# Kernel optimization log

Measured on AMD Instinct MI355X. Metric: run time of the kernel, lower is better.

## Reference

```python
import jax, jax.numpy as jnp
import numpy as np

FEATURE_DIM = 1024
HEADS = 16
HEAD_DIM = FEATURE_DIM // HEADS


def setup_inputs() -> dict:
    key = jax.random.key(0)
    ks = jax.random.split(key, 9)
    B, C, T = 4, FEATURE_DIM, 4096
    s = 1.0 / np.sqrt(C)
    inp = {
        "x": jax.random.normal(ks[0], (B, C, T), dtype=jnp.float32),
        "Wq": jax.random.uniform(ks[1], (C, C), jnp.float32, -s, s),
        "bq": jax.random.uniform(ks[2], (C,), jnp.float32, -s, s),
        "Wk": jax.random.uniform(ks[3], (C, C), jnp.float32, -s, s),
        "bk": jax.random.uniform(ks[4], (C,), jnp.float32, -s, s),
        "Wv": jax.random.uniform(ks[5], (C, C), jnp.float32, -s, s),
        "bv": jax.random.uniform(ks[6], (C,), jnp.float32, -s, s),
        "Wo": jax.random.uniform(ks[7], (C, C), jnp.float32, -s, s),
        "bo": jax.random.uniform(ks[8], (C,), jnp.float32, -s, s),
    }
    return inp


def reference(x, Wq, bq, Wk, bk, Wv, bv, Wo, bo):
    B, C, T = x.shape
    H, D = HEADS, HEAD_DIM
    xt = jnp.transpose(x, (0, 2, 1))  # [B, T, C]
    # torch Linear: y = x @ W.T + b
    q = jax.nn.elu(xt @ Wq.T + bq).reshape(B, T, H, D) + 1.0
    k = jax.nn.elu(xt @ Wk.T + bk).reshape(B, T, H, D) + 1.0
    v = (xt @ Wv.T + bv).reshape(B, T, H, D)
    kv = jnp.einsum('bthd,bthe->bhde', k, v)      # [B, H, D, D]
    z = jnp.einsum('bthd,bhd->bth', q, k.sum(axis=1))  # [B, T, H]
    num = jnp.einsum('bthd,bhde->bthe', q, kv)    # [B, T, H, D]
    out = num / (z[..., None] + 1e-6)
    out = out.reshape(B, T, C)
    out = out @ Wo.T + bo  # dropout is identity in eval mode
    return jnp.transpose(out + xt, (0, 2, 1))  # [B, C, T]
```

## Files before the change

### kernel.cpp

```cpp
#include <hip/hip_runtime.h>
#include <hip/hip_bf16.h>
#include <cmath>

typedef unsigned short u16;
typedef unsigned int   u32;

#define BB 4
#define CC 1024
#define TT 4096
#define HH 16
#define DD 64

using bf16x8 = __attribute__((ext_vector_type(8))) __bf16;
using f32x4  = __attribute__((ext_vector_type(4))) float;

union FragU { bf16x8 v; u16 u[8]; };

__device__ __forceinline__ float bf2f(u16 u) {
    union { u32 i; float f; } v; v.i = ((u32)u) << 16; return v.f;
}
__device__ __forceinline__ u16 f2bf(float f) {
    union { float f; u32 i; } v; v.f = f;
    u32 x = v.i;
    return (u16)((x + 0x7fffu + ((x >> 16) & 1u)) >> 16);
}

__device__ __forceinline__ void gl_lds16(const u16* g, u16* l) {
    __builtin_amdgcn_global_load_lds(
        (const __attribute__((address_space(1))) void*)g,
        (__attribute__((address_space(3))) void*)l, 16, 0, 0);
}

__global__ __launch_bounds__(256) void prep_kernel(
    const float* __restrict__ x,
    const float* __restrict__ Wq, const float* __restrict__ Wk,
    const float* __restrict__ Wv, const float* __restrict__ Wo,
    u16* __restrict__ xt, u16* __restrict__ Wcat, u16* __restrict__ Wob,
    float* __restrict__ kvz)
{
    __shared__ u16 tile[64 * 258];
    const int id  = blockIdx.x;
    const int tid = threadIdx.x;

    if (id < 1024) {
        const int t0 = (id & 63) * 64;
        const int c0 = ((id >> 6) & 3) * 256;
        const int b  = id >> 8;
        const float* xb  = x  + (size_t)b * CC * TT;
        u16*         xtb = xt + (size_t)b * TT * CC;
        const int tcol = tid & 63;
        const int rw   = tid >> 6;
        #pragma unroll 8
        for (int p = 0; p < 64; ++p) {
            const int cr = p * 4 + rw;
            tile[tcol * 258 + cr] = f2bf(xb[(size_t)(c0 + cr) * TT + t0 + tcol]);
        }
        __syncthreads();
        const int cp = tid & 127;
        const int th = tid >> 7;
        #pragma unroll 8
        for (int q = 0; q < 32; ++q) {
            const int tr = q * 2 + th;
            const u32 v = *reinterpret_cast<const u32*>(&tile[tr * 258 + cp * 2]);
            *reinterpret_cast<u32*>(&xtb[(size_t)(t0 + tr) * CC + c0 + cp * 2]) = v;
        }
    } else if (id < 5120) {
        const int id2  = id - 1024;
        const int wsel = id2 >> 10;
        const int i    = ((id2 & 1023) * 256 + tid) * 4;
        const float* src = (wsel == 0) ? Wq : (wsel == 1) ? Wk : (wsel == 2) ? Wv : Wo;
        u16* dst = (wsel < 3) ? (Wcat + (size_t)wsel * CC * CC) : Wob;
        const float4 v = *reinterpret_cast<const float4*>(src + i);
        ushort4 o;
        o.x = f2bf(v.x); o.y = f2bf(v.y); o.z = f2bf(v.z); o.w = f2bf(v.w);
        *reinterpret_cast<ushort4*>(dst + i) = o;
    } else {
        const int idx = ((id - 5120) * 256 + tid) * 4;
        *reinterpret_cast<float4*>(&kvz[idx]) = (float4){0.f, 0.f, 0.f, 0.f};
    }
}

template <int MODE>
__global__ __launch_bounds__(256, 2) void gemm_kernel(
    const u16* __restrict__ A, const u16* __restrict__ W,
    const float* __restrict__ b0, const float* __restrict__ b1,
    const float* __restrict__ b2, u16* __restrict__ Ybf,
    float* __restrict__ Yf, const float* __restrict__ xres,
    int M, int N, int K)
{
    __shared__ char smem[34048];
    u16* As = (u16*)smem;
    u16* Ws = (u16*)(smem + 16384);

    const int tid  = threadIdx.x;
    const int w    = tid >> 6;
    const int lane = tid & 63;
    const int wm = w >> 1, wn = w & 1;
    const int quad = lane >> 4, l16 = lane & 15;
    const int m0 = blockIdx.y * 128;
    const int n0 = blockIdx.x * 128;

    const int srow = lane >> 3;
    const int scol = ((lane & 7) ^ srow) * 8;

    f32x4 acc[4][4];
    #pragma unroll
    for (int i = 0; i < 4; ++i)
        #pragma unroll
        for (int j = 0; j < 4; ++j) acc[i][j] = (f32x4)0.0f;

    for (int k0 = 0; k0 < K; k0 += 64) {
        __syncthreads();
        #pragma unroll
        for (int s = 0; s < 4; ++s)
            gl_lds16(A + (size_t)(m0 + 32 * w + 8 * s + srow) * K + k0 + scol,
                     &As[(32 * w + 8 * s) * 64]);
        #pragma unroll
        for (int s = 0; s < 4; ++s)
            gl_lds16(W + (size_t)(n0 + 32 * w + 8 * s + srow) * K + k0 + scol,
                     &Ws[(32 * w + 8 * s) * 64]);
        __syncthreads();

        #pragma unroll
        for (int sub = 0; sub < 2; ++sub) {
            const int pg = (((sub << 2) | quad) ^ (l16 & 7)) * 8;
            bf16x8 af[4], bfr[4];
            #pragma unroll
            for (int i = 0; i < 4; ++i) {
                af[i]  = *reinterpret_cast<const bf16x8*>(&As[(wm * 64 + i * 16 + l16) * 64 + pg]);
                bfr[i] = *reinterpret_cast<const bf16x8*>(&Ws[(wn * 64 + i * 16 + l16) * 64 + pg]);
            }
            #pragma unroll
            for (int i = 0; i < 4; ++i)
                #pragma unroll
                for (int j = 0; j < 4; ++j)
                    acc[i][j] = __builtin_amdgcn_mfma_f32_16x16x32_bf16(af[i], bfr[j], acc[i][j], 0, 0, 0);
        }
    }

    if (MODE == 2) {
        float* Cs = (float*)smem;
        const int b     = m0 / TT;
        const int tbase = m0 - b * TT;
        const int cl    = lane >> 4;
        #pragma unroll
        for (int hh = 0; hh < 2; ++hh) {
            __syncthreads();
            if (wm == hh) {
                #pragma unroll
                for (int i = 0; i < 4; ++i)
                    #pragma unroll
                    for (int j = 0; j < 4; ++j)
                        #pragma unroll
                        for (int r = 0; r < 4; ++r)
                            Cs[(i * 16 + quad * 4 + r) * 133 + wn * 64 + j * 16 + l16] = acc[i][j][r];
            }
            __syncthreads();
            #pragma unroll
            for (int p = 0; p < 8; ++p) {
                const int col = p * 16 + w * 4 + cl;
                const int tl  = l16 * 4;
                float4 v;
                v.x = Cs[(tl + 0) * 133 + col];
                v.y = Cs[(tl + 1) * 133 + col];
                v.z = Cs[(tl + 2) * 133 + col];
                v.w = Cs[(tl + 3) * 133 + col];
                const float bv = b0[n0 + col];
                const size_t base = ((size_t)b * CC + n0 + col) * TT + tbase + hh * 64 + tl;
                const float4 rx = *reinterpret_cast<const float4*>(&xres[base]);
                v.x += bv + rx.x; v.y += bv + rx.y;
                v.z += bv + rx.z; v.w += bv + rx.w;
                *reinterpret_cast<float4*>(&Yf[base]) = v;
            }
        }
    } else {
        const int seg = n0 >> 10;
        const float* bp = (seg == 0) ? b0 : ((seg == 1) ? b1 : b2);
        if (seg == 0) {
            #pragma unroll
            for (int i = 0; i < 4; ++i) {
                const int row = m0 + wm * 64 + i * 16 + quad * 4;
                #pragma unroll
                for (int j = 0; j < 4; ++j) {
                    const int colL = wn * 64 + j * 16 + l16;
                    const float bv = bp[colL];
                    #pragma unroll
                    for (int r = 0; r < 4; ++r) {
                        float v = acc[i][j][r] + bv;
                        v = (v > 0.0f) ? (v + 1.0f) : __expf(v);
                        Ybf[(size_t)(row + r) * CC + colL] = f2bf(v);
                    }
                }
            }
        } else {
            u16* Yt = Ybf + (size_t)seg * M * CC;
            const int b = m0 / TT;
            #pragma unroll
            for (int i = 0; i < 4; ++i) {
                const int t = (m0 - b * TT) + wm * 64 + i * 16 + quad * 4;
                #pragma unroll
                for (int j = 0; j < 4; ++j) {
                    const int colL = (n0 & 1023) + wn * 64 + j * 16 + l16;
                    const float bv = bp[colL];
                    ushort4 o;
                    #pragma unroll
                    for (int r = 0; r < 4; ++r) {
                        float v = acc[i][j][r] + bv;
                        if (seg == 1) v = (v > 0.0f) ? (v + 1.0f) : __expf(v);
                        ((u16*)&o)[r] = f2bf(v);
                    }
                    *reinterpret_cast<ushort4*>(
                        &Yt[((size_t)(b * CC + colL)) * TT + t]) = o;
                }
            }
        }
    }
}

__global__ __launch_bounds__(256) void kv_kernel(
    const u16* __restrict__ Kt, const u16* __restrict__ Vt,
    float* __restrict__ kv, float* __restrict__ ksum)
{
    __shared__ u16 Ks[64 * 64];
    __shared__ u16 Vs[64 * 64];
    const int bh = blockIdx.x;
    const int b = bh >> 4, h = bh & 15;
    const int tc0 = blockIdx.y * 512;
    const int tid = threadIdx.x;
    const int w = tid >> 6, lane = tid & 63;
    const int quad = lane >> 4, l16 = lane & 15;

    const u16* Kg = Kt + ((size_t)(b * CC + h * DD)) * TT;
    const u16* Vg = Vt + ((size_t)(b * CC + h * DD)) * TT;

    const int srow = lane >> 3;
    const int scol = ((lane & 7) ^ srow) * 8;

    f32x4 acc[4];
    #pragma unroll
    for (int j = 0; j < 4; ++j) acc[j] = (f32x4)0.0f;
    f32x4 ks = (f32x4)0.0f;

    FragU ones;
    #pragma unroll
    for (int j = 0; j < 8; ++j) ones.u[j] = (l16 == 0) ? 0x3F80u : 0u;

    for (int it = 0; it < 8; ++it) {
        const int t0 = tc0 + it * 64;
        __syncthreads();
        #pragma unroll
        for (int s = 0; s < 2; ++s) {
            gl_lds16(Kg + (size_t)(16 * w + 8 * s + srow) * TT + t0 + scol,
                     &Ks[(16 * w + 8 * s) * 64]);
            gl_lds16(Vg + (size_t)(16 * w + 8 * s + srow) * TT + t0 + scol,
                     &Vs[(16 * w + 8 * s) * 64]);
        }
        __syncthreads();

        #pragma unroll
        for (int sub = 0; sub < 2; ++sub) {
            const int pg = (((sub << 2) | quad) ^ (l16 & 7)) * 8;
            const bf16x8 af = *reinterpret_cast<const bf16x8*>(
                &Ks[(w * 16 + l16) * 64 + pg]);
            #pragma unroll
            for (int e4 = 0; e4 < 4; ++e4) {
                const bf16x8 bfv = *reinterpret_cast<const bf16x8*>(
                    &Vs[(e4 * 16 + l16) * 64 + pg]);
                acc[e4] = __builtin_amdgcn_mfma_f32_16x16x32_bf16(af, bfv, acc[e4], 0, 0, 0);
            }
            ks = __builtin_amdgcn_mfma_f32_16x16x32_bf16(af, ones.v, ks, 0, 0, 0);
        }
    }

    float* kvb = kv + (size_t)bh * DD * DD;
    #pragma unroll
    for (int e4 = 0; e4 < 4; ++e4)
        #pragma unroll
        for (int r = 0; r < 4; ++r)
            atomicAdd(&kvb[(w * 16 + quad * 4 + r) * DD + e4 * 16 + l16], acc[e4][r]);
    if (l16 == 0) {
        #pragma unroll
        for (int r = 0; r < 4; ++r)
            atomicAdd(&ksum[bh * DD + w * 16 + quad * 4 + r], ks[r]);
    }
}

__global__ __launch_bounds__(256) void attn_kernel(
    const u16* __restrict__ Q, const float* __restrict__ kv,
    const float* __restrict__ ksum, u16* __restrict__ attn)
{
    __shared__ u16 Qs[256 * 64];
    __shared__ float kvs[DD * DD];
    __shared__ float kss[DD];
    const int bh = blockIdx.x;
    const int b = bh >> 4, h = bh & 15;
    const int tb = blockIdx.y * 256;
    const int tid = threadIdx.x;
    const int w = tid >> 6, lane = tid & 63;
    const int quad = lane >> 4, l16 = lane & 15;

    {
        const int srow = lane >> 3;
        const int scol = ((lane & 7) ^ srow) * 8;
        const u16* Qg = Q + ((size_t)(b * TT + tb)) * CC + h * DD;
        #pragma unroll
        for (int p = 0; p < 8; ++p)
            gl_lds16(Qg + (size_t)(64 * w + 8 * p + srow) * CC + scol,
                     &Qs[(64 * w + 8 * p) * 64]);
    }
    {
        const float4* s4 = reinterpret_cast<const float4*>(kv + (size_t)bh * DD * DD);
        float4* d4 = reinterpret_cast<float4*>(kvs);
        #pragma unroll
        for (int p = 0; p < 4; ++p) d4[p * 256 + tid] = s4[p * 256 + tid];
        if (tid < DD) kss[tid] = ksum[bh * DD + tid];
    }
    __syncthreads();

    FragU bf[4][2], zb[2];
    #pragma unroll
    for (int ck = 0; ck < 2; ++ck) {
        #pragma unroll
        for (int nt = 0; nt < 4; ++nt)
            #pragma unroll
            for (int j = 0; j < 8; ++j)
                bf[nt][ck].u[j] = f2bf(kvs[(ck * 32 + quad * 8 + j) * DD + nt * 16 + l16]);
        #pragma unroll
        for (int j = 0; j < 8; ++j)
            zb[ck].u[j] = (l16 == 0) ? f2bf(kss[ck * 32 + quad * 8 + j]) : 0u;
    }

    f32x4 acc[4][4], zacc[4];
    #pragma unroll
    for (int i = 0; i < 4; ++i) {
        zacc[i] = (f32x4)0.0f;
        #pragma unroll
        for (int j = 0; j < 4; ++j) acc[i][j] = (f32x4)0.0f;
    }

    #pragma unroll
    for (int i = 0; i < 4; ++i) {
        const int trow = w * 64 + i * 16 + l16;
        #pragma unroll
        for (int ck = 0; ck < 2; ++ck) {
            const int pg = (((ck << 2) | quad) ^ (l16 & 7)) * 8;
            const bf16x8 af = *reinterpret_cast<const bf16x8*>(&Qs[trow * 64 + pg]);
            #pragma unroll
            for (int nt = 0; nt < 4; ++nt)
                acc[i][nt] = __builtin_amdgcn_mfma_f32_16x16x32_bf16(af, bf[nt][ck].v, acc[i][nt], 0, 0, 0);
            zacc[i] = __builtin_amdgcn_mfma_f32_16x16x32_bf16(af, zb[ck].v, zacc[i], 0, 0, 0);
        }
    }

    u16* obase = attn + ((size_t)b * TT) * CC + h * DD;
    #pragma unroll
    for (int i = 0; i < 4; ++i) {
        float inv[4];
        #pragma unroll
        for (int r = 0; r < 4; ++r) {
            const float zv = __shfl(zacc[i][r], lane & 48);
            inv[r] = 1.0f / (zv + 1e-6f);
        }
        #pragma unroll
        for (int nt = 0; nt < 4; ++nt) {
            #pragma unroll
            for (int r = 0; r < 4; ++r) {
                const int t = tb + w * 64 + i * 16 + quad * 4 + r;
                obase[(size_t)t * CC + nt * 16 + l16] = f2bf(acc[i][nt][r] * inv[r]);
            }
        }
    }
}

extern "C" void kernel_launch(void* const* d_in, const int* in_sizes, int n_in,
                              void* d_out, int out_size, void* d_ws, size_t ws_size,
                              hipStream_t stream)
{
    const float* x  = (const float*)d_in[0];
    const float* Wq = (const float*)d_in[1];
    const float* bq = (const float*)d_in[2];
    const float* Wk = (const float*)d_in[3];
    const float* bk = (const float*)d_in[4];
    const float* Wv = (const float*)d_in[5];
    const float* bv = (const float*)d_in[6];
    const float* Wo = (const float*)d_in[7];
    const float* bo = (const float*)d_in[8];
    float* out = (float*)d_out;

    const int M = BB * TT;
    const size_t BUF  = (size_t)BB * TT * CC * sizeof(u16);
    const size_t WBUF = (size_t)CC * CC * sizeof(u16);

    char* ws = (char*)d_ws;
    u16* xt   = (u16*)(ws);
    u16* Qb   = (u16*)(ws + BUF);
    u16* Wcat = (u16*)(ws + 4 * BUF);
    u16* Wob  = (u16*)(ws + 4 * BUF + 3 * WBUF);
    float* kvbuf = (float*)(ws + 4 * BUF + 4 * WBUF);
    float* ksumb = kvbuf + (size_t)BB * HH * DD * DD;
    u16* attn = xt;

    prep_kernel<<<5380, 256, 0, stream>>>(x, Wq, Wk, Wv, Wo, xt, Wcat, Wob, kvbuf);

    gemm_kernel<3><<<dim3(3 * CC / 128, M / 128), 256, 0, stream>>>(
        xt, Wcat, bq, bk, bv, Qb, nullptr, nullptr, M, 3 * CC, CC);

    kv_kernel<<<dim3(BB * HH, TT / 512), 256, 0, stream>>>(
        Qb + (size_t)M * CC, Qb + 2 * (size_t)M * CC, kvbuf, ksumb);

    attn_kernel<<<dim3(BB * HH, TT / 256), 256, 0, stream>>>(Qb, kvbuf, ksumb, attn);

    gemm_kernel<2><<<dim3(CC / 128, M / 128), 256, 0, stream>>>(
        attn, Wob, bo, nullptr, nullptr, nullptr, out, x, M, CC, CC);
}
```

Measured before the change: 339.6 us.

## Add dedicated 256x256-tile QKV GEMM kernel with pipelined direct-to-LDS loads

Replaces the generic 128x128 GEMM used for the fused QKV projection with a specialized kernel using 256x256 output tiles, 512 threads, and double-buffered LDS filled by global-to-LDS loads with XOR-swizzled layout. The main loop interleaves fragment loads, async stages and MFMA quarters with explicit barriers, waitcnts and setprio, and the block index is remapped for L2 locality. Larger tiles raise arithmetic intensity and the staged schedule aims to hide memory latency. In exchange it uses much more LDS and registers per block, which may limit occupancy, and its hand-built barrier and waitcnt schedule is fragile.

```diff
diff --git a/kernel.cpp b/kernel.cpp
--- a/kernel.cpp
+++ b/kernel.cpp
@@ -77,6 +77,182 @@
     } else {
         const int idx = ((id - 5120) * 256 + tid) * 4;
         *reinterpret_cast<float4*>(&kvz[idx]) = (float4){0.f, 0.f, 0.f, 0.f};
+    }
+}
+
+__device__ __forceinline__ bf16x8 ldfrag(const u16* Xs, int row, int kk, int quad, int l7) {
+    return *reinterpret_cast<const bf16x8*>(&Xs[row * 64 + ((((kk << 2) | quad) ^ l7) << 3)]);
+}
+
+__global__ __launch_bounds__(512, 2) void qkv_kernel(
+    const u16* __restrict__ A, const u16* __restrict__ W,
+    const float* __restrict__ bq, const float* __restrict__ bk,
+    const float* __restrict__ bv, u16* __restrict__ Ybf)
+{
+    __shared__ __align__(16) u16 As[2][256 * 64];
+    __shared__ __align__(16) u16 Bs[2][256 * 64];
+
+    const int tid  = threadIdx.x;
+    const int w    = tid >> 6;
+    const int lane = tid & 63;
+    const int wm   = w >> 2;
+    const int wn   = w & 3;
+    const int quad = lane >> 4;
+    const int l16  = lane & 15;
+    const int l7   = l16 & 7;
+
+    const int bid = blockIdx.x;
+    const int wg  = (bid & 7) * 96 + (bid >> 3);
+    const int m0  = (wg / 12) * 256;
+    const int n0  = (wg % 12) * 256;
+
+    const u16* Ag = A + (size_t)m0 * CC;
+    const u16* Wg = W + (size_t)n0 * CC;
+
+    const int r8 = lane >> 3;
+    const int cg = ((lane & 7) ^ r8) * 8;
+
+#define STG(Xg, Xs, h, kt)                                                          \
+    { _Pragma("unroll")                                                             \
+      for (int s_ = 0; s_ < 2; ++s_)                                                \
+        gl_lds16((Xg) + (size_t)((h) * 128 + w * 16 + s_ * 8 + r8) * CC             \
+                     + (kt) * 64 + cg,                                              \
+                 &(Xs)[((h) * 128 + w * 16 + s_ * 8) * 64]); }
+
+#define BAR() { asm volatile("" ::: "memory"); __builtin_amdgcn_s_barrier(); \
+                asm volatile("" ::: "memory"); }
+
+    STG(Ag, As[0], 0, 0); STG(Ag, As[0], 1, 0);
+    STG(Wg, Bs[0], 0, 0); STG(Wg, Bs[0], 1, 0);
+    STG(Ag, As[1], 0, 1); STG(Ag, As[1], 1, 1);
+    STG(Wg, Bs[1], 0, 1);
+    asm volatile("s_waitcnt vmcnt(6)" ::: "memory");
+    BAR();
+
+    f32x4 acc[8][4];
+    #pragma unroll
+    for (int i = 0; i < 8; ++i)
+        #pragma unroll
+        for (int jj = 0; jj < 4; ++jj) acc[i][jj] = (f32x4)0.0f;
+
+    bf16x8 af[2][4][2];
+    bf16x8 bfr[2][2];
+
+#define LOAD_A(MH, CUR)                                                             \
+    { _Pragma("unroll")                                                             \
+      for (int i_ = 0; i_ < 4; ++i_)                                                \
+        _Pragma("unroll")                                                           \
+        for (int kk_ = 0; kk_ < 2; ++kk_)                                           \
+          af[MH][i_][kk_] = ldfrag(&As[CUR][0],                                     \
+              wm * 128 + (MH) * 64 + i_ * 16 + l16, kk_, quad, l7); }
+
+#define LOAD_B(NH, CUR)                                                             \
+    { _Pragma("unroll")                                                             \
+      for (int jl_ = 0; jl_ < 2; ++jl_)                                             \
+        _Pragma("unroll")                                                           \
+        for (int kk_ = 0; kk_ < 2; ++kk_)                                           \
+          bfr[jl_][kk_] = ldfrag(&Bs[CUR][0],                                       \
+              wn * 64 + ((NH) * 2 + jl_) * 16 + l16, kk_, quad, l7); }
+
+#define MFMA_Q(MH, NH)                                                              \
+    { __builtin_amdgcn_s_setprio(1);                                                \
+      _Pragma("unroll")                                                             \
+      for (int kk_ = 0; kk_ < 2; ++kk_)                                             \
+        _Pragma("unroll")                                                           \
+        for (int i_ = 0; i_ < 4; ++i_)                                              \
+          _Pragma("unroll")                                                         \
+          for (int jl_ = 0; jl_ < 2; ++jl_)                                         \
+            acc[(MH) * 4 + i_][(NH) * 2 + jl_] =                                    \
+              __builtin_amdgcn_mfma_f32_16x16x32_bf16(af[MH][i_][kk_],              \
+                  bfr[jl_][kk_], acc[(MH) * 4 + i_][(NH) * 2 + jl_], 0, 0, 0);      \
+      __builtin_amdgcn_s_setprio(0); }
+
+#define BLOCK(CUR, NXT, J, DO_S0, DO_S23, VM)                                       \
+  {                                                                                 \
+                            \
+    LOAD_A(0, CUR); LOAD_B(0, CUR);                                                 \
+    if (DO_S0) { STG(Wg, Bs[NXT], 1, (J) + 1); }                                    \
+    BAR();                                                                          \
+    asm volatile("s_waitcnt lgkmcnt(0)" ::: "memory");                              \
+    MFMA_Q(0, 0);                                                                   \
+    BAR();                                                                          \
+                                                              \
+    LOAD_A(1, CUR);                                                                 \
+    BAR();                                                                          \
+    asm volatile("s_waitcnt lgkmcnt(0)" ::: "memory");                              \
+    MFMA_Q(1, 0);                                                                   \
+    BAR();                                                                          \
+                                     \
+    LOAD_B(1, CUR);                                                                 \
+    if (DO_S23) { STG(Ag, As[CUR], 0, (J) + 2); }                                   \
+    BAR();                                                                          \
+    asm volatile("s_waitcnt lgkmcnt(0)" ::: "memory");                              \
+    MFMA_Q(0, 1);                                                                   \
+    BAR();                                                                          \
+                       \
+    if (DO_S23) { STG(Ag, As[CUR], 1, (J) + 2); STG(Wg, Bs[CUR], 0, (J) + 2); }     \
+    BAR();                                                                          \
+    MFMA_Q(1, 1);                                                                   \
+    if ((VM) == 6)      { asm volatile("s_waitcnt vmcnt(6)" ::: "memory"); }        \
+    else if ((VM) == 0) { asm volatile("s_waitcnt vmcnt(0)" ::: "memory"); }        \
+    BAR();                                                                          \
+  }
+
+    for (int j = 0; j < 14; j += 2) {
+        BLOCK(0, 1, j,     1, 1, 6);
+        BLOCK(1, 0, j + 1, 1, 1, 6);
+    }
+    BLOCK(0, 1, 14, 1, 0, 0);
+    BLOCK(1, 0, 15, 0, 0, -1);
+
+#undef BLOCK
+#undef MFMA_Q
+#undef LOAD_B
+#undef LOAD_A
+#undef BAR
+#undef STG
+
+    const int seg = n0 >> 10;
+    const int nL  = n0 & 1023;
+    if (seg == 0) {
+        #pragma unroll
+        for (int i = 0; i < 8; ++i) {
+            const int row = m0 + wm * 128 + i * 16 + quad * 4;
+            #pragma unroll
+            for (int jj = 0; jj < 4; ++jj) {
+                const int col = nL + wn * 64 + jj * 16 + l16;
+                const float bvs = bq[col];
+                #pragma unroll
+                for (int r = 0; r < 4; ++r) {
+                    float v = acc[i][jj][r] + bvs;
+                    v = (v > 0.0f) ? (v + 1.0f) : __expf(v);
+                    Ybf[(size_t)(row + r) * CC + col] = f2bf(v);
+                }
+            }
+        }
+    } else {
+        const float* bp = (seg == 1) ? bk : bv;
+        u16* Yt = Ybf + (size_t)seg * (size_t)(BB * TT) * CC;
+        const int b  = m0 / TT;
+        const int tb = m0 - b * TT + wm * 128;
+        #pragma unroll
+        for (int i = 0; i < 8; ++i) {
+            const int t = tb + i * 16 + quad * 4;
+            #pragma unroll
+            for (int jj = 0; jj < 4; ++jj) {
+                const int col = nL + wn * 64 + jj * 16 + l16;
+                const float bvs = bp[col];
+                ushort4 o;
+                #pragma unroll
+                for (int r = 0; r < 4; ++r) {
+                    float v = acc[i][jj][r] + bvs;
+                    if (seg == 1) v = (v > 0.0f) ? (v + 1.0f) : __expf(v);
+                    ((u16*)&o)[r] = f2bf(v);
+                }
+                *reinterpret_cast<ushort4*>(
+                    &Yt[((size_t)(b * CC + col)) * TT + t]) = o;
+            }
+        }
     }
 }
 
@@ -173,47 +349,6 @@
                 *reinterpret_cast<float4*>(&Yf[base]) = v;
             }
         }
-    } else {
-        const int seg = n0 >> 10;
-        const float* bp = (seg == 0) ? b0 : ((seg == 1) ? b1 : b2);
-        if (seg == 0) {
-            #pragma unroll
-            for (int i = 0; i < 4; ++i) {
-                const int row = m0 + wm * 64 + i * 16 + quad * 4;
-                #pragma unroll
-                for (int j = 0; j < 4; ++j) {
-                    const int colL = wn * 64 + j * 16 + l16;
-                    const float bv = bp[colL];
-                    #pragma unroll
-                    for (int r = 0; r < 4; ++r) {
-                        float v = acc[i][j][r] + bv;
-                        v = (v > 0.0f) ? (v + 1.0f) : __expf(v);
-                        Ybf[(size_t)(row + r) * CC + colL] = f2bf(v);
-                    }
-                }
-            }
-        } else {
-            u16* Yt = Ybf + (size_t)seg * M * CC;
-            const int b = m0 / TT;
-            #pragma unroll
-            for (int i = 0; i < 4; ++i) {
-                const int t = (m0 - b * TT) + wm * 64 + i * 16 + quad * 4;
-                #pragma unroll
-                for (int j = 0; j < 4; ++j) {
-                    const int colL = (n0 & 1023) + wn * 64 + j * 16 + l16;
-                    const float bv = bp[colL];
-                    ushort4 o;
-                    #pragma unroll
-                    for (int r = 0; r < 4; ++r) {
-                        float v = acc[i][j][r] + bv;
-                        if (seg == 1) v = (v > 0.0f) ? (v + 1.0f) : __expf(v);
-                        ((u16*)&o)[r] = f2bf(v);
-                    }
-                    *reinterpret_cast<ushort4*>(
-                        &Yt[((size_t)(b * CC + colL)) * TT + t]) = o;
-                }
-            }
-        }
     }
 }
 
@@ -402,8 +537,7 @@
 
     prep_kernel<<<5380, 256, 0, stream>>>(x, Wq, Wk, Wv, Wo, xt, Wcat, Wob, kvbuf);
 
-    gemm_kernel<3><<<dim3(3 * CC / 128, M / 128), 256, 0, stream>>>(
-        xt, Wcat, bq, bk, bv, Qb, nullptr, nullptr, M, 3 * CC, CC);
+    qkv_kernel<<<768, 512, 0, stream>>>(xt, Wcat, bq, bk, bv, Qb);
 
     kv_kernel<<<dim3(BB * HH, TT / 512), 256, 0, stream>>>(
         Qb + (size_t)M * CC, Qb + 2 * (size_t)M * CC, kvbuf, ksumb);
```

After: 357.8 us. 1.05x slower.

## Double-buffer KV loads and stage attention output through LDS for coalesced stores

Applied to the files above, without the earlier changes.

The kv kernel now double-buffers its K/V LDS tiles, issuing the next tile's global-to-LDS load before computing on the current one so load latency overlaps the MFMA work. The attention kernel writes its normalized output into the Q shared tile first and then stores it to global memory as 16-byte vectors per thread, replacing scattered 2-byte stores. This uses twice the LDS in kv_kernel and adds extra barriers in attn_kernel.

```diff
diff --git a/kernel.cpp b/kernel.cpp
--- a/kernel.cpp
+++ b/kernel.cpp
@@ -221,8 +221,8 @@
     const u16* __restrict__ Kt, const u16* __restrict__ Vt,
     float* __restrict__ kv, float* __restrict__ ksum)
 {
-    __shared__ u16 Ks[64 * 64];
-    __shared__ u16 Vs[64 * 64];
+    __shared__ u16 Ks[2][64 * 64];
+    __shared__ u16 Vs[2][64 * 64];
     const int bh = blockIdx.x;
     const int b = bh >> 4, h = bh & 15;
     const int tc0 = blockIdx.y * 512;
@@ -236,6 +236,14 @@
     const int srow = lane >> 3;
     const int scol = ((lane & 7) ^ srow) * 8;
 
+#define KVSTG(BUF, T0)                                                              \
+    { _Pragma("unroll")                                                             \
+      for (int s_ = 0; s_ < 2; ++s_) {                                              \
+        gl_lds16(Kg + (size_t)(16 * w + 8 * s_ + srow) * TT + (T0) + scol,          \
+                 &Ks[BUF][(16 * w + 8 * s_) * 64]);                                 \
+        gl_lds16(Vg + (size_t)(16 * w + 8 * s_ + srow) * TT + (T0) + scol,          \
+                 &Vs[BUF][(16 * w + 8 * s_) * 64]); } }
+
     f32x4 acc[4];
     #pragma unroll
     for (int j = 0; j < 4; ++j) acc[j] = (f32x4)0.0f;
@@ -245,32 +253,32 @@
     #pragma unroll
     for (int j = 0; j < 8; ++j) ones.u[j] = (l16 == 0) ? 0x3F80u : 0u;
 
+    KVSTG(0, tc0);
+    asm volatile("s_waitcnt vmcnt(0)" ::: "memory");
+    __syncthreads();
+
     for (int it = 0; it < 8; ++it) {
-        const int t0 = tc0 + it * 64;
-        __syncthreads();
-        #pragma unroll
-        for (int s = 0; s < 2; ++s) {
-            gl_lds16(Kg + (size_t)(16 * w + 8 * s + srow) * TT + t0 + scol,
-                     &Ks[(16 * w + 8 * s) * 64]);
-            gl_lds16(Vg + (size_t)(16 * w + 8 * s + srow) * TT + t0 + scol,
-                     &Vs[(16 * w + 8 * s) * 64]);
-        }
-        __syncthreads();
+        const int cur = it & 1;
+        if (it < 7) KVSTG(cur ^ 1, tc0 + (it + 1) * 64);
 
         #pragma unroll
         for (int sub = 0; sub < 2; ++sub) {
             const int pg = (((sub << 2) | quad) ^ (l16 & 7)) * 8;
             const bf16x8 af = *reinterpret_cast<const bf16x8*>(
-                &Ks[(w * 16 + l16) * 64 + pg]);
+                &Ks[cur][(w * 16 + l16) * 64 + pg]);
             #pragma unroll
             for (int e4 = 0; e4 < 4; ++e4) {
                 const bf16x8 bfv = *reinterpret_cast<const bf16x8*>(
-                    &Vs[(e4 * 16 + l16) * 64 + pg]);
+                    &Vs[cur][(e4 * 16 + l16) * 64 + pg]);
                 acc[e4] = __builtin_amdgcn_mfma_f32_16x16x32_bf16(af, bfv, acc[e4], 0, 0, 0);
             }
             ks = __builtin_amdgcn_mfma_f32_16x16x32_bf16(af, ones.v, ks, 0, 0, 0);
         }
-    }
+
+        asm volatile("s_waitcnt vmcnt(0)" ::: "memory");
+        __syncthreads();
+    }
+#undef KVSTG
 
     float* kvb = kv + (size_t)bh * DD * DD;
     #pragma unroll
@@ -352,7 +360,8 @@
         }
     }
 
-    u16* obase = attn + ((size_t)b * TT) * CC + h * DD;
+    __syncthreads();
+    u16* Sb = Qs;
     #pragma unroll
     for (int i = 0; i < 4; ++i) {
         float inv[4];
@@ -362,13 +371,21 @@
             inv[r] = 1.0f / (zv + 1e-6f);
         }
         #pragma unroll
-        for (int nt = 0; nt < 4; ++nt) {
-            #pragma unroll
-            for (int r = 0; r < 4; ++r) {
-                const int t = tb + w * 64 + i * 16 + quad * 4 + r;
-                obase[(size_t)t * CC + nt * 16 + l16] = f2bf(acc[i][nt][r] * inv[r]);
-            }
-        }
+        for (int nt = 0; nt < 4; ++nt)
+            #pragma unroll
+            for (int r = 0; r < 4; ++r)
+                Sb[(w * 64 + i * 16 + quad * 4 + r) * 64 + nt * 16 + l16] =
+                    f2bf(acc[i][nt][r] * inv[r]);
+    }
+    __syncthreads();
+
+    u16* obase = attn + ((size_t)b * TT + tb) * CC + h * DD;
+    #pragma unroll
+    for (int p = 0; p < 8; ++p) {
+        const int tl = p * 32 + (tid >> 3);
+        const int c8 = (tid & 7) * 8;
+        const uint4 v = *reinterpret_cast<const uint4*>(&Sb[tl * 64 + c8]);
+        *reinterpret_cast<uint4*>(&obase[(size_t)tl * CC + c8]) = v;
     }
 }
 
```

Result: slower. 349.2 us (+2.8%).

## Fuse K/V projection with kv reduction and Q projection with attention apply

Applied to the files above, without the earlier changes.

Replaces the single QKV GEMM plus separate kv and attention kernels with two fused kernels. One computes K and V tiles in registers, applies ELU and bias, stages them in LDS and immediately reduces them into per-head kv and ksum via atomics, so K and V never go to global memory. The other computes Q tiles and applies the kv matrix and normalizer in the epilogue, writing the attention output directly. The aim is to cut large intermediate HBM traffic and launches. The cost is heavier register pressure and 64KB LDS in the KV kernel, which may lower occupancy, plus more atomic traffic from many tiles.

```diff
diff --git a/kernel.cpp b/kernel.cpp
--- a/kernel.cpp
+++ b/kernel.cpp
@@ -77,6 +77,288 @@
     } else {
         const int idx = ((id - 5120) * 256 + tid) * 4;
         *reinterpret_cast<float4*>(&kvz[idx]) = (float4){0.f, 0.f, 0.f, 0.f};
+    }
+}
+
+__global__ __launch_bounds__(256, 2) void kvfuse_kernel(
+    const u16* __restrict__ A, const u16* __restrict__ Wk,
+    const u16* __restrict__ Wv, const float* __restrict__ bk,
+    const float* __restrict__ bv, float* __restrict__ kv,
+    float* __restrict__ ksum)
+{
+    __shared__ __align__(16) char smem[65536];
+    u16* As  = (u16*)smem;
+    u16* WKs = (u16*)(smem + 16384);
+    u16* WVs = (u16*)(smem + 32768);
+
+    const int tid  = threadIdx.x;
+    const int w    = tid >> 6;
+    const int lane = tid & 63;
+    const int wm = w >> 1, wn = w & 1;
+    const int quad = lane >> 4, l16 = lane & 15;
+    const int n0 = blockIdx.x * 128;
+    const int m0 = blockIdx.y * 128;
+
+    const int srow = lane >> 3;
+    const int scol = ((lane & 7) ^ srow) * 8;
+
+    f32x4 ak[4][4], av[4][4];
+    #pragma unroll
+    for (int i = 0; i < 4; ++i)
+        #pragma unroll
+        for (int j = 0; j < 4; ++j) { ak[i][j] = (f32x4)0.0f; av[i][j] = (f32x4)0.0f; }
+
+    for (int k0 = 0; k0 < CC; k0 += 64) {
+        __syncthreads();
+        #pragma unroll
+        for (int s = 0; s < 4; ++s) {
+            gl_lds16(A  + (size_t)(m0 + 32 * w + 8 * s + srow) * CC + k0 + scol,
+                     &As [(32 * w + 8 * s) * 64]);
+            gl_lds16(Wk + (size_t)(n0 + 32 * w + 8 * s + srow) * CC + k0 + scol,
+                     &WKs[(32 * w + 8 * s) * 64]);
+            gl_lds16(Wv + (size_t)(n0 + 32 * w + 8 * s + srow) * CC + k0 + scol,
+                     &WVs[(32 * w + 8 * s) * 64]);
+        }
+        __syncthreads();
+
+        #pragma unroll
+        for (int sub = 0; sub < 2; ++sub) {
+            const int pg = (((sub << 2) | quad) ^ (l16 & 7)) * 8;
+            bf16x8 af[4], bk4[4], bv4[4];
+            #pragma unroll
+            for (int i = 0; i < 4; ++i) {
+                af[i]  = *reinterpret_cast<const bf16x8*>(&As [(wm * 64 + i * 16 + l16) * 64 + pg]);
+                bk4[i] = *reinterpret_cast<const bf16x8*>(&WKs[(wn * 64 + i * 16 + l16) * 64 + pg]);
+                bv4[i] = *reinterpret_cast<const bf16x8*>(&WVs[(wn * 64 + i * 16 + l16) * 64 + pg]);
+            }
+            #pragma unroll
+            for (int i = 0; i < 4; ++i)
+                #pragma unroll
+                for (int j = 0; j < 4; ++j) {
+                    ak[i][j] = __builtin_amdgcn_mfma_f32_16x16x32_bf16(af[i], bk4[j], ak[i][j], 0, 0, 0);
+                    av[i][j] = __builtin_amdgcn_mfma_f32_16x16x32_bf16(af[i], bv4[j], av[i][j], 0, 0, 0);
+                }
+        }
+    }
+
+    __syncthreads();
+    u16* Kl = (u16*)smem;
+    u16* Vl = (u16*)(smem + 32768);
+
+    float bkk[4], bvv[4];
+    #pragma unroll
+    for (int j = 0; j < 4; ++j) {
+        bkk[j] = bk[n0 + wn * 64 + j * 16 + l16];
+        bvv[j] = bv[n0 + wn * 64 + j * 16 + l16];
+    }
+    #pragma unroll
+    for (int i = 0; i < 4; ++i) {
+        const int t4 = wm * 64 + i * 16 + quad * 4;
+        #pragma unroll
+        for (int j = 0; j < 4; ++j) {
+            const int c    = wn * 64 + j * 16 + l16;
+            const int toff = t4 ^ ((c & 15) * 8);
+            ushort4 oK, oV;
+            #pragma unroll
+            for (int r = 0; r < 4; ++r) {
+                float vK = ak[i][j][r] + bkk[j];
+                vK = (vK > 0.0f) ? (vK + 1.0f) : __expf(vK);
+                ((u16*)&oK)[r] = f2bf(vK);
+                ((u16*)&oV)[r] = f2bf(av[i][j][r] + bvv[j]);
+            }
+            *reinterpret_cast<ushort4*>(&Kl[c * 128 + toff]) = oK;
+            *reinterpret_cast<ushort4*>(&Vl[c * 128 + toff]) = oV;
+        }
+    }
+    __syncthreads();
+
+    const int hh    = w >> 1;
+    const int dbase = (w & 1) * 32;
+    const int b     = m0 >> 12;
+    const int bh    = b * HH + blockIdx.x * 2 + hh;
+
+    FragU ones;
+    #pragma unroll
+    for (int j = 0; j < 8; ++j) ones.u[j] = (l16 == 0) ? 0x3F80u : 0u;
+
+    f32x4 ckv[2][4], cks[2];
+    #pragma unroll
+    for (int s = 0; s < 2; ++s) {
+        cks[s] = (f32x4)0.0f;
+        #pragma unroll
+        for (int e4 = 0; e4 < 4; ++e4) ckv[s][e4] = (f32x4)0.0f;
+    }
+
+    #pragma unroll
+    for (int kt = 0; kt < 4; ++kt) {
+        const int tg = kt * 32 + quad * 8;
+        #pragma unroll
+        for (int s = 0; s < 2; ++s) {
+            const int ca = hh * 64 + dbase + s * 16 + l16;
+            const bf16x8 af = *reinterpret_cast<const bf16x8*>(
+                &Kl[ca * 128 + (tg ^ (l16 * 8))]);
+            #pragma unroll
+            for (int e4 = 0; e4 < 4; ++e4) {
+                const int cb = hh * 64 + e4 * 16 + l16;
+                const bf16x8 bfv = *reinterpret_cast<const bf16x8*>(
+                    &Vl[cb * 128 + (tg ^ (l16 * 8))]);
+                ckv[s][e4] = __builtin_amdgcn_mfma_f32_16x16x32_bf16(af, bfv, ckv[s][e4], 0, 0, 0);
+            }
+            cks[s] = __builtin_amdgcn_mfma_f32_16x16x32_bf16(af, ones.v, cks[s], 0, 0, 0);
+        }
+    }
+
+    float* kvb = kv + (size_t)bh * DD * DD;
+    #pragma unroll
+    for (int s = 0; s < 2; ++s)
+        #pragma unroll
+        for (int e4 = 0; e4 < 4; ++e4)
+            #pragma unroll
+            for (int r = 0; r < 4; ++r)
+                atomicAdd(&kvb[(dbase + s * 16 + quad * 4 + r) * DD + e4 * 16 + l16],
+                          ckv[s][e4][r]);
+    if (l16 == 0) {
+        #pragma unroll
+        for (int s = 0; s < 2; ++s)
+            #pragma unroll
+            for (int r = 0; r < 4; ++r)
+                atomicAdd(&ksum[bh * DD + dbase + s * 16 + quad * 4 + r], cks[s][r]);
+    }
+}
+
+__global__ __launch_bounds__(256, 2) void qattn_kernel(
+    const u16* __restrict__ A, const u16* __restrict__ Wq,
+    const float* __restrict__ bq, const float* __restrict__ kv,
+    const float* __restrict__ ksum, u16* __restrict__ attnO)
+{
+    __shared__ __align__(16) char smem[32768];
+    u16* As = (u16*)smem;
+    u16* Ws = (u16*)(smem + 16384);
+
+    const int tid  = threadIdx.x;
+    const int w    = tid >> 6;
+    const int lane = tid & 63;
+    const int wm = w >> 1, wn = w & 1;
+    const int quad = lane >> 4, l16 = lane & 15;
+    const int l7 = l16 & 7;
+    const int n0 = blockIdx.x * 128;
+    const int m0 = blockIdx.y * 128;
+
+    const int srow = lane >> 3;
+    const int scol = ((lane & 7) ^ srow) * 8;
+
+    f32x4 acc[4][4];
+    #pragma unroll
+    for (int i = 0; i < 4; ++i)
+        #pragma unroll
+        for (int j = 0; j < 4; ++j) acc[i][j] = (f32x4)0.0f;
+
+    for (int k0 = 0; k0 < CC; k0 += 64) {
+        __syncthreads();
+        #pragma unroll
+        for (int s = 0; s < 4; ++s) {
+            gl_lds16(A  + (size_t)(m0 + 32 * w + 8 * s + srow) * CC + k0 + scol,
+                     &As[(32 * w + 8 * s) * 64]);
+            gl_lds16(Wq + (size_t)(n0 + 32 * w + 8 * s + srow) * CC + k0 + scol,
+                     &Ws[(32 * w + 8 * s) * 64]);
+        }
+        __syncthreads();
+
+        #pragma unroll
+        for (int sub = 0; sub < 2; ++sub) {
+            const int pg = (((sub << 2) | quad) ^ l7) * 8;
+            bf16x8 af[4], bfr[4];
+            #pragma unroll
+            for (int i = 0; i < 4; ++i) {
+                af[i]  = *reinterpret_cast<const bf16x8*>(&As[(wm * 64 + i * 16 + l16) * 64 + pg]);
+                bfr[i] = *reinterpret_cast<const bf16x8*>(&Ws[(wn * 64 + i * 16 + l16) * 64 + pg]);
+            }
+            #pragma unroll
+            for (int i = 0; i < 4; ++i)
+                #pragma unroll
+                for (int j = 0; j < 4; ++j)
+                    acc[i][j] = __builtin_amdgcn_mfma_f32_16x16x32_bf16(af[i], bfr[j], acc[i][j], 0, 0, 0);
+        }
+    }
+
+    __syncthreads();
+    u16* Qt = (u16*)smem;
+    float bqq[4];
+    #pragma unroll
+    for (int j = 0; j < 4; ++j) bqq[j] = bq[n0 + wn * 64 + j * 16 + l16];
+    #pragma unroll
+    for (int i = 0; i < 4; ++i) {
+        #pragma unroll
+        for (int j = 0; j < 4; ++j) {
+            const int c = wn * 64 + j * 16 + l16;
+            #pragma unroll
+            for (int r = 0; r < 4; ++r) {
+                const int t = wm * 64 + i * 16 + quad * 4 + r;
+                float v = acc[i][j][r] + bqq[j];
+                v = (v > 0.0f) ? (v + 1.0f) : __expf(v);
+                Qt[t * 128 + (c ^ ((t & 7) * 8))] = f2bf(v);
+            }
+        }
+    }
+    __syncthreads();
+
+    const int hh = w >> 1, th = w & 1;
+    const int b  = m0 >> 12;
+    const int bh = b * HH + blockIdx.x * 2 + hh;
+    const float* kvh = kv + (size_t)bh * DD * DD;
+
+    FragU bf[4][2], zb[2];
+    #pragma unroll
+    for (int ck = 0; ck < 2; ++ck) {
+        #pragma unroll
+        for (int nt = 0; nt < 4; ++nt)
+            #pragma unroll
+            for (int j = 0; j < 8; ++j)
+                bf[nt][ck].u[j] = f2bf(kvh[(ck * 32 + quad * 8 + j) * DD + nt * 16 + l16]);
+        #pragma unroll
+        for (int j = 0; j < 8; ++j)
+            zb[ck].u[j] = (l16 == 0) ? f2bf(ksum[bh * DD + ck * 32 + quad * 8 + j]) : 0u;
+    }
+
+    f32x4 a2[4][4], za[4];
+    #pragma unroll
+    for (int i = 0; i < 4; ++i) {
+        za[i] = (f32x4)0.0f;
+        #pragma unroll
+        for (int j = 0; j < 4; ++j) a2[i][j] = (f32x4)0.0f;
+    }
+
+    #pragma unroll
+    for (int i = 0; i < 4; ++i) {
+        const int trow = th * 64 + i * 16 + l16;
+        #pragma unroll
+        for (int ck = 0; ck < 2; ++ck) {
+            const bf16x8 af = *reinterpret_cast<const bf16x8*>(
+                &Qt[trow * 128 + (((hh * 8 + ck * 4 + quad) ^ l7) * 8)]);
+            #pragma unroll
+            for (int nt = 0; nt < 4; ++nt)
+                a2[i][nt] = __builtin_amdgcn_mfma_f32_16x16x32_bf16(af, bf[nt][ck].v, a2[i][nt], 0, 0, 0);
+            za[i] = __builtin_amdgcn_mfma_f32_16x16x32_bf16(af, zb[ck].v, za[i], 0, 0, 0);
+        }
+    }
+
+    #pragma unroll
+    for (int i = 0; i < 4; ++i) {
+        float inv[4];
+        #pragma unroll
+        for (int r = 0; r < 4; ++r) {
+            const float zv = __shfl(za[i][r], lane & 48);
+            inv[r] = 1.0f / (zv + 1e-6f);
+        }
+        #pragma unroll
+        for (int nt = 0; nt < 4; ++nt) {
+            #pragma unroll
+            for (int r = 0; r < 4; ++r) {
+                const size_t row = (size_t)(m0 + th * 64 + i * 16 + quad * 4 + r);
+                const int    col = n0 + hh * 64 + nt * 16 + l16;
+                attnO[row * CC + col] = f2bf(a2[i][nt][r] * inv[r]);
+            }
+        }
     }
 }
 
@@ -173,202 +455,6 @@
                 *reinterpret_cast<float4*>(&Yf[base]) = v;
             }
         }
-    } else {
-        const int seg = n0 >> 10;
-        const float* bp = (seg == 0) ? b0 : ((seg == 1) ? b1 : b2);
-        if (seg == 0) {
-            #pragma unroll
-            for (int i = 0; i < 4; ++i) {
-                const int row = m0 + wm * 64 + i * 16 + quad * 4;
-                #pragma unroll
-                for (int j = 0; j < 4; ++j) {
-                    const int colL = wn * 64 + j * 16 + l16;
-                    const float bv = bp[colL];
-                    #pragma unroll
-                    for (int r = 0; r < 4; ++r) {
-                        float v = acc[i][j][r] + bv;
-                        v = (v > 0.0f) ? (v + 1.0f) : __expf(v);
-                        Ybf[(size_t)(row + r) * CC + colL] = f2bf(v);
-                    }
-                }
-            }
-        } else {
-            u16* Yt = Ybf + (size_t)seg * M * CC;
-            const int b = m0 / TT;
-            #pragma unroll
-            for (int i = 0; i < 4; ++i) {
-                const int t = (m0 - b * TT) + wm * 64 + i * 16 + quad * 4;
-                #pragma unroll
-                for (int j = 0; j < 4; ++j) {
-                    const int colL = (n0 & 1023) + wn * 64 + j * 16 + l16;
-                    const float bv = bp[colL];
-                    ushort4 o;
-                    #pragma unroll
-                    for (int r = 0; r < 4; ++r) {
-                        float v = acc[i][j][r] + bv;
-                        if (seg == 1) v = (v > 0.0f) ? (v + 1.0f) : __expf(v);
-                        ((u16*)&o)[r] = f2bf(v);
-                    }
-                    *reinterpret_cast<ushort4*>(
-                        &Yt[((size_t)(b * CC + colL)) * TT + t]) = o;
-                }
-            }
-        }
-    }
-}
-
-__global__ __launch_bounds__(256) void kv_kernel(
-    const u16* __restrict__ Kt, const u16* __restrict__ Vt,
-    float* __restrict__ kv, float* __restrict__ ksum)
-{
-    __shared__ u16 Ks[64 * 64];
-    __shared__ u16 Vs[64 * 64];
-    const int bh = blockIdx.x;
-    const int b = bh >> 4, h = bh & 15;
-    const int tc0 = blockIdx.y * 512;
-    const int tid = threadIdx.x;
-    const int w = tid >> 6, lane = tid & 63;
-    const int quad = lane >> 4, l16 = lane & 15;
-
-    const u16* Kg = Kt + ((size_t)(b * CC + h * DD)) * TT;
-    const u16* Vg = Vt + ((size_t)(b * CC + h * DD)) * TT;
-
-    const int srow = lane >> 3;
-    const int scol = ((lane & 7) ^ srow) * 8;
-
-    f32x4 acc[4];
-    #pragma unroll
-    for (int j = 0; j < 4; ++j) acc[j] = (f32x4)0.0f;
-    f32x4 ks = (f32x4)0.0f;
-
-    FragU ones;
-    #pragma unroll
-    for (int j = 0; j < 8; ++j) ones.u[j] = (l16 == 0) ? 0x3F80u : 0u;
-
-    for (int it = 0; it < 8; ++it) {
-        const int t0 = tc0 + it * 64;
-        __syncthreads();
-        #pragma unroll
-        for (int s = 0; s < 2; ++s) {
-            gl_lds16(Kg + (size_t)(16 * w + 8 * s + srow) * TT + t0 + scol,
-                     &Ks[(16 * w + 8 * s) * 64]);
-            gl_lds16(Vg + (size_t)(16 * w + 8 * s + srow) * TT + t0 + scol,
-                     &Vs[(16 * w + 8 * s) * 64]);
-        }
-        __syncthreads();
-
-        #pragma unroll
-        for (int sub = 0; sub < 2; ++sub) {
-            const int pg = (((sub << 2) | quad) ^ (l16 & 7)) * 8;
-            const bf16x8 af = *reinterpret_cast<const bf16x8*>(
-                &Ks[(w * 16 + l16) * 64 + pg]);
-            #pragma unroll
-            for (int e4 = 0; e4 < 4; ++e4) {
-                const bf16x8 bfv = *reinterpret_cast<const bf16x8*>(
-                    &Vs[(e4 * 16 + l16) * 64 + pg]);
-                acc[e4] = __builtin_amdgcn_mfma_f32_16x16x32_bf16(af, bfv, acc[e4], 0, 0, 0);
-            }
-            ks = __builtin_amdgcn_mfma_f32_16x16x32_bf16(af, ones.v, ks, 0, 0, 0);
-        }
-    }
-
-    float* kvb = kv + (size_t)bh * DD * DD;
-    #pragma unroll
-    for (int e4 = 0; e4 < 4; ++e4)
-        #pragma unroll
-        for (int r = 0; r < 4; ++r)
-            atomicAdd(&kvb[(w * 16 + quad * 4 + r) * DD + e4 * 16 + l16], acc[e4][r]);
-    if (l16 == 0) {
-        #pragma unroll
-        for (int r = 0; r < 4; ++r)
-            atomicAdd(&ksum[bh * DD + w * 16 + quad * 4 + r], ks[r]);
-    }
-}
-
-__global__ __launch_bounds__(256) void attn_kernel(
-    const u16* __restrict__ Q, const float* __restrict__ kv,
-    const float* __restrict__ ksum, u16* __restrict__ attn)
-{
-    __shared__ u16 Qs[256 * 64];
-    __shared__ float kvs[DD * DD];
-    __shared__ float kss[DD];
-    const int bh = blockIdx.x;
-    const int b = bh >> 4, h = bh & 15;
-    const int tb = blockIdx.y * 256;
-    const int tid = threadIdx.x;
-    const int w = tid >> 6, lane = tid & 63;
-    const int quad = lane >> 4, l16 = lane & 15;
-
-    {
-        const int srow = lane >> 3;
-        const int scol = ((lane & 7) ^ srow) * 8;
-        const u16* Qg = Q + ((size_t)(b * TT + tb)) * CC + h * DD;
-        #pragma unroll
-        for (int p = 0; p < 8; ++p)
-            gl_lds16(Qg + (size_t)(64 * w + 8 * p + srow) * CC + scol,
-                     &Qs[(64 * w + 8 * p) * 64]);
-    }
-    {
-        const float4* s4 = reinterpret_cast<const float4*>(kv + (size_t)bh * DD * DD);
-        float4* d4 = reinterpret_cast<float4*>(kvs);
-        #pragma unroll
-        for (int p = 0; p < 4; ++p) d4[p * 256 + tid] = s4[p * 256 + tid];
-        if (tid < DD) kss[tid] = ksum[bh * DD + tid];
-    }
-    __syncthreads();
-
-    FragU bf[4][2], zb[2];
-    #pragma unroll
-    for (int ck = 0; ck < 2; ++ck) {
-        #pragma unroll
-        for (int nt = 0; nt < 4; ++nt)
-            #pragma unroll
-            for (int j = 0; j < 8; ++j)
-                bf[nt][ck].u[j] = f2bf(kvs[(ck * 32 + quad * 8 + j) * DD + nt * 16 + l16]);
-        #pragma unroll
-        for (int j = 0; j < 8; ++j)
-            zb[ck].u[j] = (l16 == 0) ? f2bf(kss[ck * 32 + quad * 8 + j]) : 0u;
-    }
-
-    f32x4 acc[4][4], zacc[4];
-    #pragma unroll
-    for (int i = 0; i < 4; ++i) {
-        zacc[i] = (f32x4)0.0f;
-        #pragma unroll
-        for (int j = 0; j < 4; ++j) acc[i][j] = (f32x4)0.0f;
-    }
-
-    #pragma unroll
-    for (int i = 0; i < 4; ++i) {
-        const int trow = w * 64 + i * 16 + l16;
-        #pragma unroll
-        for (int ck = 0; ck < 2; ++ck) {
-            const int pg = (((ck << 2) | quad) ^ (l16 & 7)) * 8;
-            const bf16x8 af = *reinterpret_cast<const bf16x8*>(&Qs[trow * 64 + pg]);
-            #pragma unroll
-            for (int nt = 0; nt < 4; ++nt)
-                acc[i][nt] = __builtin_amdgcn_mfma_f32_16x16x32_bf16(af, bf[nt][ck].v, acc[i][nt], 0, 0, 0);
-            zacc[i] = __builtin_amdgcn_mfma_f32_16x16x32_bf16(af, zb[ck].v, zacc[i], 0, 0, 0);
-        }
-    }
-
-    u16* obase = attn + ((size_t)b * TT) * CC + h * DD;
-    #pragma unroll
-    for (int i = 0; i < 4; ++i) {
-        float inv[4];
-        #pragma unroll
-        for (int r = 0; r < 4; ++r) {
-            const float zv = __shfl(zacc[i][r], lane & 48);
-            inv[r] = 1.0f / (zv + 1e-6f);
-        }
-        #pragma unroll
-        for (int nt = 0; nt < 4; ++nt) {
-            #pragma unroll
-            for (int r = 0; r < 4; ++r) {
-                const int t = tb + w * 64 + i * 16 + quad * 4 + r;
-                obase[(size_t)t * CC + nt * 16 + l16] = f2bf(acc[i][nt][r] * inv[r]);
-            }
-        }
     }
 }
 
@@ -398,18 +484,15 @@
     u16* Wob  = (u16*)(ws + 4 * BUF + 3 * WBUF);
     float* kvbuf = (float*)(ws + 4 * BUF + 4 * WBUF);
     float* ksumb = kvbuf + (size_t)BB * HH * DD * DD;
-    u16* attn = xt;
 
     prep_kernel<<<5380, 256, 0, stream>>>(x, Wq, Wk, Wv, Wo, xt, Wcat, Wob, kvbuf);
 
-    gemm_kernel<3><<<dim3(3 * CC / 128, M / 128), 256, 0, stream>>>(
-        xt, Wcat, bq, bk, bv, Qb, nullptr, nullptr, M, 3 * CC, CC);
-
-    kv_kernel<<<dim3(BB * HH, TT / 512), 256, 0, stream>>>(
-        Qb + (size_t)M * CC, Qb + 2 * (size_t)M * CC, kvbuf, ksumb);
-
-    attn_kernel<<<dim3(BB * HH, TT / 256), 256, 0, stream>>>(Qb, kvbuf, ksumb, attn);
+    kvfuse_kernel<<<dim3(CC / 128, M / 128), 256, 0, stream>>>(
+        xt, Wcat + (size_t)CC * CC, Wcat + 2 * (size_t)CC * CC, bk, bv, kvbuf, ksumb);
+
+    qattn_kernel<<<dim3(CC / 128, M / 128), 256, 0, stream>>>(
+        xt, Wcat, bq, kvbuf, ksumb, Qb);
 
     gemm_kernel<2><<<dim3(CC / 128, M / 128), 256, 0, stream>>>(
-        attn, Wob, bo, nullptr, nullptr, nullptr, out, x, M, CC, CC);
-}
+        Qb, Wob, bo, nullptr, nullptr, nullptr, out, x, M, CC, CC);
+}
```

After: 337.6 us. No clear change (-0.6%).
